# Kernel optimization log

Measured on AMD Instinct MI355X. Metric: run time of the kernel, lower is better.

## Reference

```python
import jax, jax.numpy as jnp
import numpy as np

EPS = 1e-5  # InstanceNorm2d default eps (affine=False, biased var)

def setup_inputs() -> dict:
    key = jax.random.key(0)
    ks = jax.random.split(key, 16)
    B, N, KV, H = 16, 196, 960, 4
    chs = [64, 128, 256, 512]
    inp = {}
    inp['emb0'] = jax.random.normal(ks[0], (B, N, chs[0]), jnp.float32)
    inp['emb1'] = jax.random.normal(ks[1], (B, N, chs[1]), jnp.float32)
    inp['emb2'] = jax.random.normal(ks[2], (B, N, chs[2]), jnp.float32)
    inp['emb3'] = jax.random.normal(ks[3], (B, N, chs[3]), jnp.float32)
    inp['emb_all'] = jax.random.normal(ks[4], (B, N, KV), jnp.float32)
    for i, ch in enumerate(chs):
        inp[f'Wq{i}'] = jax.random.normal(ks[5 + i], (H, ch, ch), jnp.float32) * (1.0 / np.sqrt(ch))
        inp[f'Wo{i}'] = jax.random.normal(ks[9 + i], (ch, ch), jnp.float32) * (1.0 / np.sqrt(ch))
    inp['Wk'] = jax.random.normal(ks[13], (H, KV, KV), jnp.float32) * (1.0 / np.sqrt(KV))
    inp['Wv'] = jax.random.normal(ks[14], (H, KV, KV), jnp.float32) * (1.0 / np.sqrt(KV))
    return inp

def _attend(emb, Wq, Wo, K, V, inv_sqrt_kv):
    # Q: per-head Linear(ch,ch) then transpose(-1,-2) -> [B,H,ch,N]
    Q = jnp.einsum('bnc,hdc->bhdn', emb, Wq)
    # scores: [B,H,ch,KV]
    scores = jnp.einsum('bhdn,bhnj->bhdj', Q, K) * inv_sqrt_kv
    # InstanceNorm2d over the (ch, KV) plane per (batch, head), no affine
    m = scores.mean(axis=(-2, -1), keepdims=True)
    v = scores.var(axis=(-2, -1), keepdims=True)
    probs = jax.nn.softmax((scores - m) * jax.lax.rsqrt(v + EPS), axis=-1)
    # ctx = (probs @ V^T).permute(0,3,2,1).mean(dim=3) -> mean over heads: [B,N,ch]
    ctx = jnp.einsum('bhdj,bhnj->bnd', probs, V) / probs.shape[1]
    # out projection: nn.Linear(ch,ch) -> x @ Wo^T
    return jnp.einsum('bnd,ed->bne', ctx, Wo)

def reference(emb0, emb1, emb2, emb3, emb_all, Wq0, Wq1, Wq2, Wq3, Wk, Wv, Wo0, Wo1, Wo2, Wo3):
    KV = emb_all.shape[-1]
    inv_sqrt_kv = jnp.float32(1.0 / np.sqrt(KV))
    # multi-head K/V: stacked per-head Linear(KV,KV) -> [B,H,N,KV]
    K = jnp.einsum('bnk,hjk->bhnj', emb_all, Wk)
    V = jnp.einsum('bnk,hjk->bhnj', emb_all, Wv)
    o0 = _attend(emb0, Wq0, Wo0, K, V, inv_sqrt_kv)
    o1 = _attend(emb1, Wq1, Wo1, K, V, inv_sqrt_kv)
    o2 = _attend(emb2, Wq2, Wo2, K, V, inv_sqrt_kv)
    o3 = _attend(emb3, Wq3, Wo3, K, V, inv_sqrt_kv)
    return (o0, o1, o2, o3)
```

## Files before the change

kernel.cpp:

```cpp
#include <hip/hip_runtime.h>

typedef _Float16 half_t;
typedef _Float16 h8 __attribute__((ext_vector_type(8)));
typedef _Float16 h4 __attribute__((ext_vector_type(4)));
typedef float f4v __attribute__((ext_vector_type(4)));

__device__ __forceinline__ int div196(int m) { return (m * 21400) >> 22; }

__device__ __forceinline__ void async16(half_t* l, const half_t* g)
{
    __builtin_amdgcn_global_load_lds(
        (const __attribute__((address_space(1))) void*)g,
        (__attribute__((address_space(3))) void*)l,
        16, 0, 0);
}

struct PrepArgs {
    const float* src[15];
    half_t* dst[15];
    int n[15];
    int mode[15];
    int lg2[15];
};

__global__ __launch_bounds__(256) void prep_k(PrepArgs a)
{
    const int seg = blockIdx.y;
    const int i8 = (blockIdx.x * 256 + threadIdx.x) * 8;
    if (i8 >= a.n[seg]) return;
    const float* s = a.src[seg] + i8;
    f4v v0 = *(const f4v*)s;
    f4v v1 = *(const f4v*)(s + 4);
    h8 o;
    o[0] = (half_t)v0[0]; o[1] = (half_t)v0[1]; o[2] = (half_t)v0[2]; o[3] = (half_t)v0[3];
    o[4] = (half_t)v1[0]; o[5] = (half_t)v1[1]; o[6] = (half_t)v1[2]; o[7] = (half_t)v1[3];
    if (a.mode[seg] == 0) {
        *(h8*)(a.dst[seg] + i8) = o;
    } else {
        const int lg = a.lg2[seg], ch = 1 << lg;
        const int e = i8 >> lg, d = i8 & (ch - 1);
        half_t* base = a.dst[seg] + ((long long)e << (lg + 2)) + d;
        #pragma unroll
        for (int r = 0; r < 4; ++r) *(h8*)(base + r * ch) = o;
    }
}

__device__ __forceinline__ h8 ldtile(const half_t* __restrict__ base, int row, int kb,
                                     int ld, int rowLim, int Klim)
{
    h8 v = {0, 0, 0, 0, 0, 0, 0, 0};
    if (row >= rowLim) return v;
    const half_t* p = base + (long long)row * ld + kb;
    if (kb + 8 <= Klim) return *(const h8*)p;
    #pragma unroll
    for (int e = 0; e < 8; ++e) if (kb + e < Klim) v[e] = p[e];
    return v;
}

struct BP {
    const half_t* A[6]; const half_t* B[6]; void* C[6];
    int Mlim[6], Nlim[6], Klim[6], nKt[6], lda[6], ldb[6], ldc[6];
    int divA[6]; long long sAhi[6], sAlo[6];
    int divB[6]; long long sBhi[6], sBlo[6];
    int divC[6]; long long sChi[6], sClo[6];
    long long tStrB[6]; int tComp[6];
    int outMode[6];
    float alpha[6];
    int mT[6], nT[6];
    int cumEnd[5];
    int totW;
};

__global__ __launch_bounds__(128)
void gemm_b(BP P)
{
    __shared__ __align__(16) half_t SM[64 * 72];
    half_t (*As)[32] = (half_t(*)[32])SM;
    half_t (*Bs)[32] = (half_t(*)[32])(SM + 2048);

    int b = blockIdx.x;
    int s = 0, basev = 0;
    #pragma unroll
    for (int i = 0; i < 5; ++i) if (b >= P.cumEnd[i]) { s = i + 1; basev = P.cumEnd[i]; }
    b -= basev;
    const int mTl = P.mT[s], nTl = P.nT[s];
    const int mt = b % mTl;
    const int t2 = b / mTl;
    const int nt = t2 % nTl;
    const int z  = t2 / nTl;

    const half_t* A  = P.A[s] + (long long)(z / P.divA[s]) * P.sAhi[s] + (long long)(z % P.divA[s]) * P.sAlo[s];
    const half_t* Bp = P.B[s] + (long long)(z / P.divB[s]) * P.sBhi[s] + (long long)(z % P.divB[s]) * P.sBlo[s];
    const int Mlim = P.Mlim[s], Klim = P.Klim[s], nKt = P.nKt[s];
    const int lda = P.lda[s], ldb = P.ldb[s], ldc = P.ldc[s];
    const float alpha = P.alpha[s];
    const int m0 = mt * 64, n0 = nt * 64;
    const int tid = threadIdx.x;
    const int lane = tid & 63, w = tid >> 6;
    const int l15 = lane & 15, q = lane >> 4;

    const int r0 = tid >> 2, kg = tid & 3;
    const int r1 = r0 + 32;

    f4v acc[4][2];
    #pragma unroll
    for (int i = 0; i < 4; ++i)
        #pragma unroll
        for (int j = 0; j < 2; ++j) acc[i][j] = (f4v){0.f, 0.f, 0.f, 0.f};

    for (int kt = 0; kt < nKt; ++kt) {
        const int kb = kt * 32 + kg * 8;
        h8 a0 = ldtile(A, m0 + r0, kb, lda, Mlim, Klim);
        h8 a1 = ldtile(A, m0 + r1, kb, lda, Mlim, Klim);
        h8 b0 = ldtile(Bp, n0 + r0, kb, ldb, 1 << 30, Klim);
        h8 b1 = ldtile(Bp, n0 + r1, kb, ldb, 1 << 30, Klim);
        __syncthreads();
        *(h8*)&As[r0][kg * 8] = a0;
        *(h8*)&As[r1][kg * 8] = a1;
        *(h8*)&Bs[r0][kg * 8] = b0;
        *(h8*)&Bs[r1][kg * 8] = b1;
        __syncthreads();
        h8 af[4], bf[2];
        #pragma unroll
        for (int mti = 0; mti < 4; ++mti) af[mti] = *(h8*)&As[mti * 16 + l15][q * 8];
        #pragma unroll
        for (int nti = 0; nti < 2; ++nti) bf[nti] = *(h8*)&Bs[w * 32 + nti * 16 + l15][q * 8];
        #pragma unroll
        for (int mti = 0; mti < 4; ++mti)
            #pragma unroll
            for (int nti = 0; nti < 2; ++nti)
                acc[mti][nti] = __builtin_amdgcn_mfma_f32_16x16x32_f16(af[mti], bf[nti], acc[mti][nti], 0, 0, 0);
    }

    float* Cz = (float*)P.C[s] + (long long)(z / P.divC[s]) * P.sChi[s] + (long long)(z % P.divC[s]) * P.sClo[s];
    #pragma unroll
    for (int mti = 0; mti < 4; ++mti)
        #pragma unroll
        for (int r = 0; r < 4; ++r) {
            const int row = m0 + mti * 16 + q * 4 + r;
            if (row < Mlim) {
                #pragma unroll
                for (int nti = 0; nti < 2; ++nti) {
                    const int col = n0 + w * 32 + nti * 16 + l15;
                    Cz[(long long)row * ldc + col] = acc[mti][nti][r] * alpha;
                }
            }
        }
}

__global__ __launch_bounds__(256)
void gemm_w(BP P)
{
    __shared__ __align__(16) half_t SMEM[16384];

    const int per = gridDim.x >> 3;
    int wk = (blockIdx.x & 7) * per + (blockIdx.x >> 3);
    if (wk >= P.totW) return;
    int s = 0, basev = 0;
    #pragma unroll
    for (int i = 0; i < 5; ++i) if (wk >= P.cumEnd[i]) { s = i + 1; basev = P.cumEnd[i]; }
    wk -= basev;
    const int mTl = P.mT[s], nTl = P.nT[s];
    const int mt = wk % mTl;
    const int t2 = wk / mTl;
    const int nt = t2 % nTl;
    const int z  = t2 / nTl;

    const half_t* A  = P.A[s] + (long long)(z / P.divA[s]) * P.sAhi[s] + (long long)(z % P.divA[s]) * P.sAlo[s];
    const half_t* Bp = P.B[s] + (long long)(z / P.divB[s]) * P.sBhi[s] + (long long)(z % P.divB[s]) * P.sBlo[s];
    const int Mlim = P.Mlim[s], Nlim = P.Nlim[s], nKt = P.nKt[s];
    const int lda = P.lda[s], ldb = P.ldb[s], ldc = P.ldc[s];
    const float alpha = P.alpha[s];
    const int m0 = mt * 128, n0 = nt * 128;
    const int tid = threadIdx.x;
    const int lane = tid & 63, wv = tid >> 6;
    const int wm = wv & 1, wn = wv >> 1;
    const int l15 = lane & 15, q = lane >> 4;
    const int r0 = tid >> 2, kg = tid & 3;

    const int rA0 = min(m0 + r0,       Mlim - 1);
    const int rA1 = min(m0 + r0 + 64,  Mlim - 1);
    const int rB0 = min(n0 + r0,       Nlim - 1);
    const int rB1 = min(n0 + r0 + 64,  Nlim - 1);
    const half_t* gA0 = A  + (long long)rA0 * lda + kg * 8;
    const half_t* gA1 = A  + (long long)rA1 * lda + kg * 8;
    const half_t* gB0 = Bp + (long long)rB0 * ldb + kg * 8;
    const half_t* gB1 = Bp + (long long)rB1 * ldb + kg * 8;

    const int wb = wv * 512;

    f4v acc[4][4];
    #pragma unroll
    for (int i = 0; i < 4; ++i)
        #pragma unroll
        for (int j = 0; j < 4; ++j) acc[i][j] = (f4v){0.f, 0.f, 0.f, 0.f};

    auto stage = [&](int buf) {
        half_t* base = SMEM + buf * 8192;
        async16(base        + wb, gA0);
        async16(base + 2048 + wb, gA1);
        async16(base + 4096 + wb, gB0);
        async16(base + 6144 + wb, gB1);
        gA0 += 32; gA1 += 32; gB0 += 32; gB1 += 32;
    };
    auto compute = [&](int buf) {
        const half_t* As = SMEM + buf * 8192;
        const half_t* Bs = As + 4096;
        h8 af[4], bf[4];
        #pragma unroll
        for (int mi = 0; mi < 4; ++mi) af[mi] = *(const h8*)(As + (wm * 64 + mi * 16 + l15) * 32 + q * 8);
        #pragma unroll
        for (int ni = 0; ni < 4; ++ni) bf[ni] = *(const h8*)(Bs + (wn * 64 + ni * 16 + l15) * 32 + q * 8);
        #pragma unroll
        for (int mi = 0; mi < 4; ++mi)
            #pragma unroll
            for (int ni = 0; ni < 4; ++ni)
                acc[mi][ni] = __builtin_amdgcn_mfma_f32_16x16x32_f16(af[mi], bf[ni], acc[mi][ni], 0, 0, 0);
    };

    stage(0);
    __syncthreads();
    for (int kt = 0; kt < nKt; kt += 2) {
        stage(1);
        compute(0);
        __syncthreads();
        if (kt + 2 < nKt) stage(0);
        compute(1);
        __syncthreads();
    }

    if (P.outMode[s] == 1) {
        half_t* Cz = (half_t*)P.C[s] + (long long)(z / P.divC[s]) * P.sChi[s] + (long long)(z % P.divC[s]) * P.sClo[s];
        #pragma unroll
        for (int mi = 0; mi < 4; ++mi)
            #pragma unroll
            for (int r = 0; r < 4; ++r) {
                const int row = m0 + wm * 64 + mi * 16 + q * 4 + r;
                if (row < Mlim) {
                    #pragma unroll
                    for (int ni = 0; ni < 4; ++ni) {
                        const int col = n0 + wn * 64 + ni * 16 + l15;
                        if (col < Nlim) Cz[(long long)row * ldc + col] = (half_t)(acc[mi][ni][r] * alpha);
                    }
                }
            }
    } else {
        half_t (*Tt)[72] = (half_t(*)[72])SMEM;
        half_t* Cz = (half_t*)P.C[s] + (long long)(z / P.divC[s]) * P.sChi[s] + (long long)(z % P.divC[s]) * P.sClo[s];
        const long long tStrB = P.tStrB[s];
        const int jl = tid >> 1, mh = (tid & 1) * 32;
        #pragma unroll
        for (int p = 0; p < 2; ++p) {
            __syncthreads();
            if (wm == p) {
                #pragma unroll
                for (int mi = 0; mi < 4; ++mi)
                    #pragma unroll
                    for (int ni = 0; ni < 4; ++ni) {
                        h4 pk;
                        #pragma unroll
                        for (int r = 0; r < 4; ++r) pk[r] = (half_t)(acc[mi][ni][r] * alpha);
                        *(h4*)&Tt[wn * 64 + ni * 16 + l15][mi * 16 + q * 4] = pk;
                    }
            }
            __syncthreads();
            const int n = n0 + jl;
            if (n < Nlim) {
                #pragma unroll
                for (int g = 0; g < 4; ++g) {
                    const int ml = mh + g * 8;
                    const int mg = m0 + p * 64 + ml;
                    h8 v = *(h8*)&Tt[jl][ml];
                    if (P.tComp[s]) {
                        const int b0 = div196(mg), b1 = div196(mg + 7);
                        if (b0 == b1 && mg + 8 <= Mlim) {
                            half_t* rp = Cz + (long long)b0 * tStrB + (long long)n * ldc + (mg - 196 * b0);
                            h4 lo = {v[0], v[1], v[2], v[3]};
                            h4 hi = {v[4], v[5], v[6], v[7]};
                            *(h4*)rp = lo;
                            *(h4*)(rp + 4) = hi;
                        } else {
                            #pragma unroll
                            for (int e = 0; e < 8; ++e) {
                                const int m = mg + e;
                                if (m < Mlim) {
                                    const int bb = div196(m);
                                    Cz[(long long)bb * tStrB + (long long)n * ldc + (m - 196 * bb)] = v[e];
                                }
                            }
                        }
                    } else {
                        if (mg + 8 <= Mlim) {
                            *(h8*)(Cz + (long long)n * ldc + mg) = v;
                        } else {
                            #pragma unroll
                            for (int e = 0; e < 8; ++e)
                                if (mg + e < Mlim) Cz[(long long)n * ldc + mg + e] = v[e];
                        }
                    }
                }
            }
        }
    }
}

struct ScP {
    const half_t* Qt[4];
    const half_t* KT;
    half_t* C[4];
    float* Part[4];
    int Mlim[4];
    long long sA[4], sC[4];
    float alpha;
};

__global__ __launch_bounds__(256)
void gemm_s(ScP P)
{
    __shared__ __align__(16) half_t As[128][232];
    __shared__ __align__(16) half_t Bs[128][72];
    __shared__ float red[8];

    const int per = gridDim.x >> 3;
    int wk = (blockIdx.x & 7) * per + (blockIdx.x >> 3);
    const int z = wk >> 3, r = wk & 7;
    int s, mt;
    if (r < 1)      { s = 0; mt = 0; }
    else if (r < 2) { s = 1; mt = 0; }
    else if (r < 4) { s = 2; mt = r - 2; }
    else            { s = 3; mt = r - 4; }
    const int b = z >> 2, h = z & 3;

    const half_t* A = P.Qt[s] + (long long)z * P.sA[s] + (long long)mt * 128 * 208;
    const half_t* B = P.KT + (long long)h * 3194880 + (long long)b * 199680;
    const int rowLim = P.Mlim[s] - mt * 128;
    const float alpha = P.alpha;

    const int tid = threadIdx.x;
    const int lane = tid & 63, wv = tid >> 6;
    const int wm = wv & 1, wn = wv >> 1;
    const int l15 = lane & 15, q = lane >> 4;
    const int r0 = tid >> 2, kg = tid & 3;

    #pragma unroll
    for (int c = 0; c < 7; ++c) {
        const int kb = c * 32 + kg * 8;
        h8 a0 = ldtile(A, r0, kb, 208, rowLim, 196);
        h8 a1 = ldtile(A, r0 + 64, kb, 208, rowLim, 196);
        *(h8*)&As[r0][kb] = a0;
        *(h8*)&As[r0 + 64][kb] = a1;
    }

    half_t* Cz = P.C[s] + (long long)z * P.sC[s] + (long long)mt * 128 * 960;
    float sv = 0.f, qq = 0.f;

    for (int nt = 0; nt < 8; ++nt) {
        f4v acc[4][4];
        #pragma unroll
        for (int i = 0; i < 4; ++i)
            #pragma unroll
            for (int j = 0; j < 4; ++j) acc[i][j] = (f4v){0.f, 0.f, 0.f, 0.f};

        const int j0 = nt * 128;
        #pragma unroll
        for (int c2 = 0; c2 < 4; ++c2) {
            h8 b00 = ldtile(B, j0 + r0,      c2 * 64 + kg * 8,      208, 960, 196);
            h8 b01 = ldtile(B, j0 + r0,      c2 * 64 + 32 + kg * 8, 208, 960, 196);
            h8 b10 = ldtile(B, j0 + r0 + 64, c2 * 64 + kg * 8,      208, 960, 196);
            h8 b11 = ldtile(B, j0 + r0 + 64, c2 * 64 + 32 + kg * 8, 208, 960, 196);
            __syncthreads();
            *(h8*)&Bs[r0][kg * 8] = b00;
            *(h8*)&Bs[r0][32 + kg * 8] = b01;
            *(h8*)&Bs[r0 + 64][kg * 8] = b10;
            *(h8*)&Bs[r0 + 64][32 + kg * 8] = b11;
            __syncthreads();
            const int nkk = (c2 < 3) ? 2 : 1;
            for (int kk = 0; kk < nkk; ++kk) {
                const int base = c2 * 64 + kk * 32;
                h8 af[4], bf[4];
                #pragma unroll
                for (int mi = 0; mi < 4; ++mi) af[mi] = *(h8*)&As[wm * 64 + mi * 16 + l15][base + q * 8];
                #pragma unroll
                for (int ni = 0; ni < 4; ++ni) bf[ni] = *(h8*)&Bs[wn * 64 + ni * 16 + l15][kk * 32 + q * 8];
                #pragma unroll
                for (int mi = 0; mi < 4; ++mi)
                    #pragma unroll
                    for (int ni = 0; ni < 4; ++ni)
                        acc[mi][ni] = __builtin_amdgcn_mfma_f32_16x16x32_f16(af[mi], bf[ni], acc[mi][ni], 0, 0, 0);
            }
        }
        #pragma unroll
        for (int mi = 0; mi < 4; ++mi)
            #pragma unroll
            for (int rr = 0; rr < 4; ++rr) {
                const int rowl = wm * 64 + mi * 16 + q * 4 + rr;
                #pragma unroll
                for (int ni = 0; ni < 4; ++ni) {
                    const int col = j0 + wn * 64 + ni * 16 + l15;
                    const float v = acc[mi][ni][rr] * alpha;
                    sv += v; qq += v * v;
                    if (rowl < rowLim && col < 960)
                        Cz[(long long)rowl * 960 + col] = (half_t)v;
                }
            }
    }

    #pragma unroll
    for (int o = 32; o > 0; o >>= 1) {
        sv += __shfl_down(sv, o, 64);
        qq += __shfl_down(qq, o, 64);
    }
    if (lane == 0) { red[wv] = sv; red[4 + wv] = qq; }
    __syncthreads();
    if (tid == 0) {
        float* PO = P.Part[s] + (long long)z * 240 + mt * 2;
        PO[0] = red[0] + red[1] + red[2] + red[3];
        PO[1] = red[4] + red[5] + red[6] + red[7];
    }
}

struct CtxP {
    const half_t* V;
    const half_t* S[4];
    half_t* C[4];
    const float* Part[4];
    int ch[4];
    int nPart[4];
    float pinv[4];
};

__global__ __launch_bounds__(256)
void ctx_k(CtxP P)
{
    __shared__ __align__(16) half_t As[128][40];
    __shared__ __align__(16) half_t Bs[128][40];
    __shared__ float denomP[128][4];
    __shared__ float denom[128];

    const int per = gridDim.x >> 3;
    int wk = (blockIdx.x & 7) * per + (blockIdx.x >> 3);
    const int z = wk >> 4;
    const int r = wk & 15;
    int s, mt, nt;
    if (r < 2)      { s = 0; mt = r;            nt = 0; }
    else if (r < 4) { s = 1; mt = r - 2;        nt = 0; }
    else if (r < 8) { s = 2; mt = (r - 4) >> 1; nt = (r - 4) & 1; }
    else            { s = 3; mt = (r - 8) >> 2; nt = (r - 8) & 3; }
    const int b = z >> 2, h = z & 3;
    const int chS = P.ch[s];

    const float* part = P.Part[s] + (long long)z * 240;
    float Ssum = 0.f, Qsum = 0.f;
    for (int i = 0; i < P.nPart[s]; ++i) { Ssum += part[i * 2]; Qsum += part[i * 2 + 1]; }
    const float mn = Ssum * P.pinv[s];
    const float rs = rsqrtf(fmaxf(Qsum * P.pinv[s] - mn * mn, 0.f) + 1e-5f);

    const half_t* Av  = P.V + (long long)h * 3010560 + (long long)b * 188160;
    const half_t* Bsc = P.S[s] + (long long)z * 960 * chS;
    const int m0 = mt * 128, n0 = nt * 128;

    const int tid = threadIdx.x;
    const int lane = tid & 63, wv = tid >> 6;
    const int wm = wv & 1, wn = wv >> 1;
    const int l15 = lane & 15, q = lane >> 4;
    const int r0 = tid >> 2, kg = tid & 3;
    const int d0 = n0 + r0, d1 = n0 + r0 + 64;
    const bool ok0 = d0 < chS, ok1 = d1 < chS;

    f4v acc[4][4];
    #pragma unroll
    for (int i = 0; i < 4; ++i)
        #pragma unroll
        for (int j = 0; j < 4; ++j) acc[i][j] = (f4v){0.f, 0.f, 0.f, 0.f};

    float ds0 = 0.f, ds1 = 0.f;

    h8 a0n = ldtile(Av, m0 + r0, kg * 8, 960, 196, 960);
    h8 a1n = ldtile(Av, m0 + r0 + 64, kg * 8, 960, 196, 960);
    h8 s0n = {0,0,0,0,0,0,0,0}, s1n = {0,0,0,0,0,0,0,0};
    if (ok0) s0n = *(const h8*)(Bsc + (long long)d0 * 960 + kg * 8);
    if (ok1) s1n = *(const h8*)(Bsc + (long long)d1 * 960 + kg * 8);

    for (int kt = 0; kt < 30; ++kt) {
        h8 e0 = {0,0,0,0,0,0,0,0}, e1 = {0,0,0,0,0,0,0,0};
        if (ok0) {
            #pragma unroll
            for (int e = 0; e < 8; ++e) { float ev = __expf((float)s0n[e] * rs); ds0 += ev; e0[e] = (half_t)ev; }
        }
        if (ok1) {
            #pragma unroll
            for (int e = 0; e < 8; ++e) { float ev = __expf((float)s1n[e] * rs); ds1 += ev; e1[e] = (half_t)ev; }
        }
        h8 a0c = a0n, a1c = a1n;
        __syncthreads();
        *(h8*)&As[r0][kg * 8] = a0c;
        *(h8*)&As[r0 + 64][kg * 8] = a1c;
        *(h8*)&Bs[r0][kg * 8] = e0;
        *(h8*)&Bs[r0 + 64][kg * 8] = e1;
        __syncthreads();
        if (kt < 29) {
            const int kb = (kt + 1) * 32 + kg * 8;
            a0n = ldtile(Av, m0 + r0, kb, 960, 196, 960);
            a1n = ldtile(Av, m0 + r0 + 64, kb, 960, 196, 960);
            if (ok0) s0n = *(const h8*)(Bsc + (long long)d0 * 960 + kb);
            if (ok1) s1n = *(const h8*)(Bsc + (long long)d1 * 960 + kb);
        }
        h8 af[4], bf[4];
        #pragma unroll
        for (int mi = 0; mi < 4; ++mi) af[mi] = *(h8*)&As[wm * 64 + mi * 16 + l15][q * 8];
        #pragma unroll
        for (int ni = 0; ni < 4; ++ni) bf[ni] = *(h8*)&Bs[wn * 64 + ni * 16 + l15][q * 8];
        #pragma unroll
        for (int mi = 0; mi < 4; ++mi)
            #pragma unroll
            for (int ni = 0; ni < 4; ++ni)
                acc[mi][ni] = __builtin_amdgcn_mfma_f32_16x16x32_f16(af[mi], bf[ni], acc[mi][ni], 0, 0, 0);
    }

    denomP[r0][kg] = ds0;
    denomP[r0 + 64][kg] = ds1;
    __syncthreads();
    if (tid < 128) denom[tid] = denomP[tid][0] + denomP[tid][1] + denomP[tid][2] + denomP[tid][3];
    __syncthreads();

    half_t* Cz = P.C[s] + (long long)b * 784 * chS + (long long)h * chS;
    const int ldc = 4 * chS;
    #pragma unroll
    for (int ni = 0; ni < 4; ++ni) {
        const int coll = wn * 64 + ni * 16 + l15;
        const int col = n0 + coll;
        if (col < chS) {
            const float sc = 0.25f / denom[coll];
            #pragma unroll
            for (int mi = 0; mi < 4; ++mi)
                #pragma unroll
                for (int rr = 0; rr < 4; ++rr) {
                    const int row = m0 + wm * 64 + mi * 16 + q * 4 + rr;
                    if (row < 196)
                        Cz[(long long)row * ldc + col] = (half_t)(acc[mi][ni][rr] * sc);
                }
        }
    }
}

extern "C" void kernel_launch(void* const* d_in, const int* in_sizes, int n_in,
                              void* d_out, int out_size, void* d_ws, size_t ws_size,
                              hipStream_t stream)
{
    const float* emb[4]  = {(const float*)d_in[0], (const float*)d_in[1],
                            (const float*)d_in[2], (const float*)d_in[3]};
    const float* emb_all = (const float*)d_in[4];
    const float* Wq[4]   = {(const float*)d_in[5], (const float*)d_in[7],
                            (const float*)d_in[9], (const float*)d_in[11]};
    const float* Wo[4]   = {(const float*)d_in[6], (const float*)d_in[8],
                            (const float*)d_in[10], (const float*)d_in[12]};
    const float* Wk = (const float*)d_in[13];
    const float* Wv = (const float*)d_in[14];
    float* out = (float*)d_out;

    half_t* hb = (half_t*)d_ws;
    half_t* EAh = hb;
    half_t* Eh  = EAh + 3010560;
    half_t* Wkh = Eh  + 3010560;
    half_t* Wvh = Wkh + 3686400;
    half_t* Wqh = Wvh + 3686400;
    half_t* Wo4 = Wqh + 1392640;
    half_t* KT  = Wo4 + 1392640;
    half_t* Vh  = KT  + 12779520;
    half_t* QtT = Vh  + 12042240;
    half_t* Ctx = QtT + 12779520;
    half_t* Sch = Ctx + 12042240;
    float*  Part = (float*)(Sch + 58982400);

    const int  chs[4]   = {64, 128, 256, 512};
    const int  lg2c[4]  = {6, 7, 8, 9};
    const long long offE[4]   = {0, 200704, 602112, 1404928};
    const long long offQ[4]   = {0, 16384, 81920, 344064};
    const long long offQt[4]  = {0, 851968, 2555904, 5963776};
    const long long offSc[4]  = {0, 3932160, 11796480, 27525120};
    const long long offCtx[4] = {0, 802816, 2408448, 5619712};
    const long long ooff[4]   = {0, 200704, 602112, 1404928};
    const float inv_sqrt_kv = 0.03227486121839514f;

    PrepArgs pa;
    pa.src[0] = emb_all; pa.dst[0] = EAh; pa.n[0] = 3010560; pa.mode[0] = 0; pa.lg2[0] = 0;
    for (int i = 0; i < 4; ++i) {
        pa.src[1 + i] = emb[i]; pa.dst[1 + i] = Eh + offE[i];
        pa.n[1 + i] = (int)(3136LL * chs[i]); pa.mode[1 + i] = 0; pa.lg2[1 + i] = 0;
    }
    pa.src[5] = Wk; pa.dst[5] = Wkh; pa.n[5] = 3686400; pa.mode[5] = 0; pa.lg2[5] = 0;
    pa.src[6] = Wv; pa.dst[6] = Wvh; pa.n[6] = 3686400; pa.mode[6] = 0; pa.lg2[6] = 0;
    for (int i = 0; i < 4; ++i) {
        pa.src[7 + i] = Wq[i]; pa.dst[7 + i] = Wqh + offQ[i];
        pa.n[7 + i] = 4 * chs[i] * chs[i]; pa.mode[7 + i] = 0; pa.lg2[7 + i] = 0;
        pa.src[11 + i] = Wo[i]; pa.dst[11 + i] = Wo4 + offQ[i];
        pa.n[11 + i] = chs[i] * chs[i]; pa.mode[11 + i] = 1; pa.lg2[11 + i] = lg2c[i];
    }
    prep_k<<<dim3(1800, 15), 256, 0, stream>>>(pa);

    {
        BP p{};
        p.A[0] = EAh; p.B[0] = Wkh; p.C[0] = KT;
        p.Mlim[0] = 3136; p.Nlim[0] = 960; p.Klim[0] = 960; p.nKt[0] = 30;
        p.lda[0] = 960; p.ldb[0] = 960; p.ldc[0] = 208;
        p.divA[0] = 1; p.sAhi[0] = 0; p.sAlo[0] = 0;
        p.divB[0] = 1; p.sBhi[0] = 921600; p.sBlo[0] = 0;
        p.divC[0] = 1; p.sChi[0] = 3194880; p.sClo[0] = 0;
        p.tStrB[0] = 199680; p.tComp[0] = 1; p.outMode[0] = 2; p.alpha[0] = 1.0f;
        p.mT[0] = 25; p.nT[0] = 8;
        p.A[1] = EAh; p.B[1] = Wvh; p.C[1] = Vh;
        p.Mlim[1] = 3136; p.Nlim[1] = 960; p.Klim[1] = 960; p.nKt[1] = 30;
        p.lda[1] = 960; p.ldb[1] = 960; p.ldc[1] = 960;
        p.divA[1] = 1; p.sAhi[1] = 0; p.sAlo[1] = 0;
        p.divB[1] = 1; p.sBhi[1] = 921600; p.sBlo[1] = 0;
        p.divC[1] = 1; p.sChi[1] = 3010560; p.sClo[1] = 0;
        p.tStrB[1] = 0; p.tComp[1] = 0; p.outMode[1] = 1; p.alpha[1] = 1.0f;
        p.mT[1] = 25; p.nT[1] = 8;
        for (int i = 0; i < 4; ++i) {
            const int sl = 2 + i, ch = chs[i];
            p.A[sl] = Eh + offE[i]; p.B[sl] = Wqh + offQ[i]; p.C[sl] = QtT + offQt[i];
            p.Mlim[sl] = 196; p.Nlim[sl] = ch; p.Klim[sl] = ch; p.nKt[sl] = ch / 32;
            p.lda[sl] = ch; p.ldb[sl] = ch; p.ldc[sl] = 208;
            p.divA[sl] = 4; p.sAhi[sl] = 196LL * ch; p.sAlo[sl] = 0;
            p.divB[sl] = 4; p.sBhi[sl] = 0; p.sBlo[sl] = (long long)ch * ch;
            p.divC[sl] = 1; p.sChi[sl] = 208LL * ch; p.sClo[sl] = 0;
            p.tStrB[sl] = 0; p.tComp[sl] = 0; p.outMode[sl] = 2; p.alpha[sl] = 1.0f;
            p.mT[sl] = 2; p.nT[sl] = (ch + 127) / 128;
        }
        int cum = 0;
        const int blocks[6] = {800, 800, 128, 128, 256, 512};
        for (int sl = 0; sl < 6; ++sl) { cum += blocks[sl]; if (sl < 5) p.cumEnd[sl] = cum; }
        p.totW = cum;
        gemm_w<<<2624, 256, 0, stream>>>(p);
    }

    {
        ScP p{};
        for (int s = 0; s < 4; ++s) {
            p.Qt[s] = QtT + offQt[s];
            p.C[s] = Sch + offSc[s];
            p.Part[s] = Part + (long long)s * 64 * 240;
            p.Mlim[s] = chs[s];
            p.sA[s] = 208LL * chs[s];
            p.sC[s] = 960LL * chs[s];
        }
        p.KT = KT;
        p.alpha = inv_sqrt_kv;
        gemm_s<<<512, 256, 0, stream>>>(p);
    }

    {
        CtxP p{};
        p.V = Vh;
        const int nP[4] = {1, 1, 2, 4};
        for (int s = 0; s < 4; ++s) {
            p.S[s] = Sch + offSc[s];
            p.C[s] = Ctx + offCtx[s];
            p.Part[s] = Part + (long long)s * 64 * 240;
            p.ch[s] = chs[s];
            p.nPart[s] = nP[s];
            p.pinv[s] = 1.0f / (chs[s] * 960);
        }
        ctx_k<<<1024, 256, 0, stream>>>(p);
    }

    {
        BP p{};
        int cum = 0;
        for (int s = 0; s < 4; ++s) {
            const int ch = chs[s];
            p.A[s] = Ctx + offCtx[s]; p.B[s] = Wo4 + offQ[s]; p.C[s] = out + ooff[s];
            p.Mlim[s] = 196; p.Nlim[s] = ch; p.Klim[s] = 4 * ch; p.nKt[s] = ch / 8;
            p.lda[s] = 4 * ch; p.ldb[s] = 4 * ch; p.ldc[s] = ch;
            p.divA[s] = 1; p.sAhi[s] = 784LL * ch; p.sAlo[s] = 0;
            p.divB[s] = 1; p.sBhi[s] = 0; p.sBlo[s] = 0;
            p.divC[s] = 1; p.sChi[s] = 196LL * ch; p.sClo[s] = 0;
            p.tStrB[s] = 0; p.tComp[s] = 0; p.outMode[s] = 0; p.alpha[s] = 1.0f;
            p.mT[s] = 4; p.nT[s] = ch / 64;
            cum += 4 * (ch / 64) * 16;
            if (s < 3) p.cumEnd[s] = cum;
        }
        p.cumEnd[3] = p.cumEnd[4] = cum;
        p.totW = cum;
        gemm_b<<<960, 128, 0, stream>>>(p);
    }
}
```

Before: 419.9 us.

## Store K transposed in flat batch-contiguous layout with swizzled single-pass epilogue

Changes the K^T buffer layout from per-batch padded [b][j][208] to a flat [h][j][3200] layout where all batches are contiguous along the row, so the gemm_w transposed epilogue no longer needs the divide-by-196 batch split and writes full 16-byte stores. The epilogue now stages the whole 128x128 tile in LDS with an XOR swizzle and a single sync instead of two passes. The score kernel's K loads are updated to the new stride, and gemm_w gets an occupancy hint of 3 blocks per CU. Rows in the score kernel now straddle batches with a larger stride, and the tail handling relies on nfull truncation to 3200-wide rows.

```diff
diff --git a/kernel.cpp b/kernel.cpp
--- a/kernel.cpp
+++ b/kernel.cpp
@@ -4,8 +4,6 @@
 typedef _Float16 h8 __attribute__((ext_vector_type(8)));
 typedef _Float16 h4 __attribute__((ext_vector_type(4)));
 typedef float f4v __attribute__((ext_vector_type(4)));
-
-__device__ __forceinline__ int div196(int m) { return (m * 21400) >> 22; }
 
 __device__ __forceinline__ void async16(half_t* l, const half_t* g)
 {
@@ -63,7 +61,6 @@
     int divA[6]; long long sAhi[6], sAlo[6];
     int divB[6]; long long sBhi[6], sBlo[6];
     int divC[6]; long long sChi[6], sClo[6];
-    long long tStrB[6]; int tComp[6];
     int outMode[6];
     float alpha[6];
     int mT[6], nT[6];
@@ -148,7 +145,7 @@
         }
 }
 
-__global__ __launch_bounds__(256)
+__global__ __launch_bounds__(256, 3)
 void gemm_w(BP P)
 {
     __shared__ __align__(16) half_t SMEM[16384];
@@ -245,59 +242,33 @@
                 }
             }
     } else {
-        half_t (*Tt)[72] = (half_t(*)[72])SMEM;
+        half_t (*T2)[128] = (half_t(*)[128])SMEM;
         half_t* Cz = (half_t*)P.C[s] + (long long)(z / P.divC[s]) * P.sChi[s] + (long long)(z % P.divC[s]) * P.sClo[s];
-        const long long tStrB = P.tStrB[s];
-        const int jl = tid >> 1, mh = (tid & 1) * 32;
-        #pragma unroll
-        for (int p = 0; p < 2; ++p) {
-            __syncthreads();
-            if (wm == p) {
+        #pragma unroll
+        for (int mi = 0; mi < 4; ++mi)
+            #pragma unroll
+            for (int ni = 0; ni < 4; ++ni) {
+                h4 pk;
                 #pragma unroll
-                for (int mi = 0; mi < 4; ++mi)
-                    #pragma unroll
-                    for (int ni = 0; ni < 4; ++ni) {
-                        h4 pk;
-                        #pragma unroll
-                        for (int r = 0; r < 4; ++r) pk[r] = (half_t)(acc[mi][ni][r] * alpha);
-                        *(h4*)&Tt[wn * 64 + ni * 16 + l15][mi * 16 + q * 4] = pk;
-                    }
+                for (int r = 0; r < 4; ++r) pk[r] = (half_t)(acc[mi][ni][r] * alpha);
+                const int col = wn * 64 + ni * 16 + l15;
+                const int g   = wm * 16 + mi * 4 + q;
+                *(h4*)&T2[col][4 * (g ^ (col & 31))] = pk;
             }
-            __syncthreads();
-            const int n = n0 + jl;
-            if (n < Nlim) {
-                #pragma unroll
-                for (int g = 0; g < 4; ++g) {
-                    const int ml = mh + g * 8;
-                    const int mg = m0 + p * 64 + ml;
-                    h8 v = *(h8*)&Tt[jl][ml];
-                    if (P.tComp[s]) {
-                        const int b0 = div196(mg), b1 = div196(mg + 7);
-                        if (b0 == b1 && mg + 8 <= Mlim) {
-                            half_t* rp = Cz + (long long)b0 * tStrB + (long long)n * ldc + (mg - 196 * b0);
-                            h4 lo = {v[0], v[1], v[2], v[3]};
-                            h4 hi = {v[4], v[5], v[6], v[7]};
-                            *(h4*)rp = lo;
-                            *(h4*)(rp + 4) = hi;
-                        } else {
-                            #pragma unroll
-                            for (int e = 0; e < 8; ++e) {
-                                const int m = mg + e;
-                                if (m < Mlim) {
-                                    const int bb = div196(m);
-                                    Cz[(long long)bb * tStrB + (long long)n * ldc + (m - 196 * bb)] = v[e];
-                                }
-                            }
-                        }
-                    } else {
-                        if (mg + 8 <= Mlim) {
-                            *(h8*)(Cz + (long long)n * ldc + mg) = v;
-                        } else {
-                            #pragma unroll
-                            for (int e = 0; e < 8; ++e)
-                                if (mg + e < Mlim) Cz[(long long)n * ldc + mg + e] = v[e];
-                        }
-                    }
+        __syncthreads();
+        {
+            const int col  = tid >> 1;
+            const int coff = (tid & 1) * 64;
+            const int gb   = (tid & 1) * 16;
+            const int mbase = m0 + coff;
+            const int nfull = max(0, min(64, ldc - mbase)) >> 3;
+            if (n0 + col < Nlim && nfull > 0) {
+                half_t* rp = Cz + (long long)(n0 + col) * ldc + mbase;
+                for (int j = 0; j < nfull; ++j) {
+                    h4 lo = *(h4*)&T2[col][4 * ((gb + 2 * j)     ^ (col & 31))];
+                    h4 hi = *(h4*)&T2[col][4 * ((gb + 2 * j + 1) ^ (col & 31))];
+                    h8 v = {lo[0], lo[1], lo[2], lo[3], hi[0], hi[1], hi[2], hi[3]};
+                    *(h8*)(rp + j * 8) = v;
                 }
             }
         }
@@ -332,7 +303,7 @@
     const int b = z >> 2, h = z & 3;
 
     const half_t* A = P.Qt[s] + (long long)z * P.sA[s] + (long long)mt * 128 * 208;
-    const half_t* B = P.KT + (long long)h * 3194880 + (long long)b * 199680;
+    const half_t* B = P.KT + (long long)h * 3072000 + (long long)b * 196;
     const int rowLim = P.Mlim[s] - mt * 128;
     const float alpha = P.alpha;
 
@@ -364,10 +335,10 @@
         const int j0 = nt * 128;
         #pragma unroll
         for (int c2 = 0; c2 < 4; ++c2) {
-            h8 b00 = ldtile(B, j0 + r0,      c2 * 64 + kg * 8,      208, 960, 196);
-            h8 b01 = ldtile(B, j0 + r0,      c2 * 64 + 32 + kg * 8, 208, 960, 196);
-            h8 b10 = ldtile(B, j0 + r0 + 64, c2 * 64 + kg * 8,      208, 960, 196);
-            h8 b11 = ldtile(B, j0 + r0 + 64, c2 * 64 + 32 + kg * 8, 208, 960, 196);
+            h8 b00 = ldtile(B, j0 + r0,      c2 * 64 + kg * 8,      3200, 960, 196);
+            h8 b01 = ldtile(B, j0 + r0,      c2 * 64 + 32 + kg * 8, 3200, 960, 196);
+            h8 b10 = ldtile(B, j0 + r0 + 64, c2 * 64 + kg * 8,      3200, 960, 196);
+            h8 b11 = ldtile(B, j0 + r0 + 64, c2 * 64 + 32 + kg * 8, 3200, 960, 196);
             __syncthreads();
             *(h8*)&Bs[r0][kg * 8] = b00;
             *(h8*)&Bs[r0][32 + kg * 8] = b01;
@@ -602,11 +573,11 @@
         BP p{};
         p.A[0] = EAh; p.B[0] = Wkh; p.C[0] = KT;
         p.Mlim[0] = 3136; p.Nlim[0] = 960; p.Klim[0] = 960; p.nKt[0] = 30;
-        p.lda[0] = 960; p.ldb[0] = 960; p.ldc[0] = 208;
+        p.lda[0] = 960; p.ldb[0] = 960; p.ldc[0] = 3200;
         p.divA[0] = 1; p.sAhi[0] = 0; p.sAlo[0] = 0;
         p.divB[0] = 1; p.sBhi[0] = 921600; p.sBlo[0] = 0;
-        p.divC[0] = 1; p.sChi[0] = 3194880; p.sClo[0] = 0;
-        p.tStrB[0] = 199680; p.tComp[0] = 1; p.outMode[0] = 2; p.alpha[0] = 1.0f;
+        p.divC[0] = 1; p.sChi[0] = 3072000; p.sClo[0] = 0;
+        p.outMode[0] = 2; p.alpha[0] = 1.0f;
         p.mT[0] = 25; p.nT[0] = 8;
         p.A[1] = EAh; p.B[1] = Wvh; p.C[1] = Vh;
         p.Mlim[1] = 3136; p.Nlim[1] = 960; p.Klim[1] = 960; p.nKt[1] = 30;
@@ -614,7 +585,7 @@
         p.divA[1] = 1; p.sAhi[1] = 0; p.sAlo[1] = 0;
         p.divB[1] = 1; p.sBhi[1] = 921600; p.sBlo[1] = 0;
         p.divC[1] = 1; p.sChi[1] = 3010560; p.sClo[1] = 0;
-        p.tStrB[1] = 0; p.tComp[1] = 0; p.outMode[1] = 1; p.alpha[1] = 1.0f;
+        p.outMode[1] = 1; p.alpha[1] = 1.0f;
         p.mT[1] = 25; p.nT[1] = 8;
         for (int i = 0; i < 4; ++i) {
             const int sl = 2 + i, ch = chs[i];
@@ -624,7 +595,7 @@
             p.divA[sl] = 4; p.sAhi[sl] = 196LL * ch; p.sAlo[sl] = 0;
             p.divB[sl] = 4; p.sBhi[sl] = 0; p.sBlo[sl] = (long long)ch * ch;
             p.divC[sl] = 1; p.sChi[sl] = 208LL * ch; p.sClo[sl] = 0;
-            p.tStrB[sl] = 0; p.tComp[sl] = 0; p.outMode[sl] = 2; p.alpha[sl] = 1.0f;
+            p.outMode[sl] = 2; p.alpha[sl] = 1.0f;
             p.mT[sl] = 2; p.nT[sl] = (ch + 127) / 128;
         }
         int cum = 0;
@@ -675,7 +646,7 @@
             p.divA[s] = 1; p.sAhi[s] = 784LL * ch; p.sAlo[s] = 0;
             p.divB[s] = 1; p.sBhi[s] = 0; p.sBlo[s] = 0;
             p.divC[s] = 1; p.sChi[s] = 196LL * ch; p.sClo[s] = 0;
-            p.tStrB[s] = 0; p.tComp[s] = 0; p.outMode[s] = 0; p.alpha[s] = 1.0f;
+            p.outMode[s] = 0; p.alpha[s] = 1.0f;
             p.mT[s] = 4; p.nT[s] = ch / 64;
             cum += 4 * (ch / 64) * 16;
             if (s < 3) p.cumEnd[s] = cum;
```

After: 418.8 us. Within noise of the previous version (-0.3%).
